# Optimization experiments

Measured on AMD Instinct MI355X. Metric: run time of the kernel, lower is better.

The kernel has to match this reference:

```python
import jax, jax.numpy as jnp
import numpy as np

IM_SIZE = (32, 32)
SCALE = float(IM_SIZE[0] * IM_SIZE[1])  # sqrt((x*y)^2) = x*y


def setup_inputs() -> dict:
    key = jax.random.key(0)
    k1, k2, k3 = jax.random.split(key, 3)
    b, n, p, x, y, d = 8, 8, 64, IM_SIZE[0], IM_SIZE[1], 8
    shape = (b, n, p, x, y, d)
    return {
        "query": jax.random.normal(k1, shape, dtype=jnp.float32),
        "key": jax.random.normal(k2, shape, dtype=jnp.float32),
        "value": jax.random.normal(k3, shape, dtype=jnp.float32),
        "key_padding_mask": jnp.zeros((b, p), dtype=bool),
    }


def reference(query, key, value, key_padding_mask):
    # scores: contract over spatial (x,y) and channel (d) dims -> [b,n,p,q]
    scores = jnp.einsum('bnpxyd,bnqxyd->bnpq', query, key) / SCALE
    if key_padding_mask is not None:
        mask = key_padding_mask[:, None, None, :]  # [b,1,1,q]
        scores = jnp.where(mask, -jnp.inf, scores)
    attn = jax.nn.softmax(scores, axis=-1)  # [b,n,p,q]
    out = jnp.einsum('bnpq,bnqxyd->bnpxyd', attn, value)
    # permute(0,2,3,4,5,1) -> [b,p,x,y,d,n]
    return jnp.transpose(out, (0, 2, 3, 4, 5, 1))
```

## Files before the change

### kernel.cpp

```cpp
#include <hip/hip_runtime.h>
#include <hip/hip_bf16.h>
#include <cstdint>
#include <cstddef>


typedef __attribute__((ext_vector_type(4))) float f32x4;
typedef __attribute__((ext_vector_type(8))) short bf16x8;
typedef __attribute__((ext_vector_type(4))) short shortx4;

__device__ __forceinline__ unsigned short f2bf(float x) {
    unsigned int u = __builtin_bit_cast(unsigned int, x);
    u += 0x7FFFu + ((u >> 16) & 1u);
    return (unsigned short)(u >> 16);
}

__global__ __launch_bounds__(256) void qk_mfma_kernel(
    const float* __restrict__ Q, const float* __restrict__ K,
    float* __restrict__ partial, int clen)
{
    const int bn   = blockIdx.x;
    const int ch   = blockIdx.y;
    const int tid  = threadIdx.x;
    const int w    = tid >> 6;
    const int lane = tid & 63;
    const int wr   = w >> 1;
    const int wc   = w & 1;
    const int frow = lane & 15;
    const int kg   = lane >> 4;

    const float* Qb = Q + (size_t)bn * 64 * 8192 + (size_t)ch * clen;
    const float* Kb = K + (size_t)bn * 64 * 8192 + (size_t)ch * clen;
    const float* Aq = Qb + (size_t)(wr * 32 + frow) * 8192 + kg * 8;
    const float* Bk = Kb + (size_t)(wc * 32 + frow) * 8192 + kg * 8;

    f32x4 acc[2][2];
    #pragma unroll
    for (int mt = 0; mt < 2; ++mt)
        #pragma unroll
        for (int nt = 0; nt < 2; ++nt)
            acc[mt][nt] = (f32x4)(0.f);

    #pragma unroll 2
    for (int ks = 0; ks < clen; ks += 32) {
        bf16x8 afr[2], bfr[2];
        #pragma unroll
        for (int mt = 0; mt < 2; ++mt) {
            const float* p = Aq + (size_t)mt * 16 * 8192 + ks;
            const float4 lo = *(const float4*)p;
            const float4 hi = *(const float4*)(p + 4);
            bf16x8 f;
            f[0] = (short)f2bf(lo.x); f[1] = (short)f2bf(lo.y);
            f[2] = (short)f2bf(lo.z); f[3] = (short)f2bf(lo.w);
            f[4] = (short)f2bf(hi.x); f[5] = (short)f2bf(hi.y);
            f[6] = (short)f2bf(hi.z); f[7] = (short)f2bf(hi.w);
            afr[mt] = f;
        }
        #pragma unroll
        for (int nt = 0; nt < 2; ++nt) {
            const float* p = Bk + (size_t)nt * 16 * 8192 + ks;
            const float4 lo = *(const float4*)p;
            const float4 hi = *(const float4*)(p + 4);
            bf16x8 f;
            f[0] = (short)f2bf(lo.x); f[1] = (short)f2bf(lo.y);
            f[2] = (short)f2bf(lo.z); f[3] = (short)f2bf(lo.w);
            f[4] = (short)f2bf(hi.x); f[5] = (short)f2bf(hi.y);
            f[6] = (short)f2bf(hi.z); f[7] = (short)f2bf(hi.w);
            bfr[nt] = f;
        }
        #pragma unroll
        for (int mt = 0; mt < 2; ++mt)
            #pragma unroll
            for (int nt = 0; nt < 2; ++nt)
                acc[mt][nt] = __builtin_amdgcn_mfma_f32_16x16x32_bf16(
                    afr[mt], bfr[nt], acc[mt][nt], 0, 0, 0);
    }

    float* pb = partial + ((size_t)ch * 64 + bn) * 4096;
    #pragma unroll
    for (int mt = 0; mt < 2; ++mt)
        #pragma unroll
        for (int nt = 0; nt < 2; ++nt) {
            const int p0 = wr * 32 + mt * 16 + kg * 4;
            const int q0 = wc * 32 + nt * 16 + frow;
            #pragma unroll
            for (int r = 0; r < 4; ++r)
                pb[(size_t)(p0 + r) * 64 + q0] = acc[mt][nt][r];
        }
}

__global__ __launch_bounds__(256) void softmax_kernel(
    float* __restrict__ ws, const unsigned char* __restrict__ mask, int kchunks)
{
    const int row  = blockIdx.x * 4 + (threadIdx.x >> 6);
    const int q    = threadIdx.x & 63;
    float s = 0.f;
    for (int c = 0; c < kchunks; ++c)
        s += ws[((size_t)c * 4096 + row) * 64 + q];
    s *= (1.0f / 1024.0f);
    const int b = row >> 9;
    if (mask[b * 64 + q]) s = -__builtin_inff();
    float m = s;
    #pragma unroll
    for (int off = 32; off; off >>= 1) m = fmaxf(m, __shfl_xor(m, off));
    const float e = __expf(s - m);
    float sum = e;
    #pragma unroll
    for (int off = 32; off; off >>= 1) sum += __shfl_xor(sum, off);
    ws[(size_t)row * 64 + q] = e / sum;
}

__global__ __launch_bounds__(512, 2) void pv_mfma_kernel(
    const float* __restrict__ V, const float* __restrict__ attn,
    float* __restrict__ out)
{
    __shared__ unsigned char smem[65536];

    const int b     = blockIdx.y;
    const int chunk = blockIdx.x;
    const int tid   = threadIdx.x;
    const int w     = tid >> 6;
    const int lane  = tid & 63;

    const float* Vb = V    + (size_t)(b * 8 + w) * 64 * 8192 + (size_t)chunk * 64;
    const float* Ab = attn + (size_t)(b * 8 + w) * 4096;

    unsigned short* vtn = (unsigned short*)smem + w * 4096;

    const int c  = lane >> 2;
    const int qg = lane & 3;
    #pragma unroll
    for (int s = 0; s < 4; ++s) {
        const int q0 = s * 16 + qg * 4;
        const float4 r0 = *(const float4*)&Vb[(size_t)(q0 + 0) * 8192 + c * 4];
        const float4 r1 = *(const float4*)&Vb[(size_t)(q0 + 1) * 8192 + c * 4];
        const float4 r2 = *(const float4*)&Vb[(size_t)(q0 + 2) * 8192 + c * 4];
        const float4 r3 = *(const float4*)&Vb[(size_t)(q0 + 3) * 8192 + c * 4];
        const float v0[4] = {r0.x, r0.y, r0.z, r0.w};
        const float v1[4] = {r1.x, r1.y, r1.z, r1.w};
        const float v2[4] = {r2.x, r2.y, r2.z, r2.w};
        const float v3[4] = {r3.x, r3.y, r3.z, r3.w};
        #pragma unroll
        for (int cc = 0; cc < 4; ++cc) {
            const int row = c * 4 + cc;
            shortx4 pk;
            pk.x = (short)f2bf(v0[cc]);
            pk.y = (short)f2bf(v1[cc]);
            pk.z = (short)f2bf(v2[cc]);
            pk.w = (short)f2bf(v3[cc]);
            const int soff = row * 64 + (q0 ^ ((row & 7) << 3) ^ (((row >> 3) & 3) << 4));
            *(shortx4*)(vtn + soff) = pk;
        }
    }

    const int arow = lane & 15;
    const int q0a  = (lane >> 4) * 8;
    bf16x8 afrag[4][2];
    #pragma unroll
    for (int mt = 0; mt < 4; ++mt) {
        #pragma unroll
        for (int ks = 0; ks < 2; ++ks) {
            const float* ap = Ab + (mt * 16 + arow) * 64 + ks * 32 + q0a;
            const float4 lo = *(const float4*)ap;
            const float4 hi = *(const float4*)(ap + 4);
            bf16x8 f;
            f[0] = (short)f2bf(lo.x); f[1] = (short)f2bf(lo.y);
            f[2] = (short)f2bf(lo.z); f[3] = (short)f2bf(lo.w);
            f[4] = (short)f2bf(hi.x); f[5] = (short)f2bf(hi.y);
            f[6] = (short)f2bf(hi.z); f[7] = (short)f2bf(hi.w);
            afrag[mt][ks] = f;
        }
    }

    f32x4 acc[4][4];
    #pragma unroll
    for (int mt = 0; mt < 4; ++mt)
        #pragma unroll
        for (int nt = 0; nt < 4; ++nt)
            acc[mt][nt] = (f32x4)(0.f);

    const int bcol = lane & 15;
    const int q0b  = (lane >> 4) * 8;
    #pragma unroll
    for (int nt = 0; nt < 4; ++nt) {
        bf16x8 bfr[2];
        #pragma unroll
        for (int ks = 0; ks < 2; ++ks) {
            const int row  = nt * 16 + bcol;
            const int q0   = ks * 32 + q0b;
            const int soff = row * 64 + (q0 ^ ((row & 7) << 3) ^ (((row >> 3) & 3) << 4));
            bfr[ks] = *(const bf16x8*)(vtn + soff);
        }
        #pragma unroll
        for (int ks = 0; ks < 2; ++ks)
            #pragma unroll
            for (int mt = 0; mt < 4; ++mt)
                acc[mt][nt] = __builtin_amdgcn_mfma_f32_16x16x32_bf16(
                    afrag[mt][ks], bfr[ks], acc[mt][nt], 0, 0, 0);
    }

    float* ob = (float*)smem;
    const int pq = lane >> 4;
    const int pl = tid >> 5;
    const int g  = tid & 31;
    #pragma unroll
    for (int mt = 0; mt < 4; ++mt) {
        __syncthreads();
        #pragma unroll
        for (int nt = 0; nt < 4; ++nt)
            #pragma unroll
            for (int r = 0; r < 4; ++r) {
                const int prow = pq * 4 + r;
                const int xc   = nt * 16 + (lane & 15);
                ob[prow * 576 + xc * 9 + w] = acc[mt][nt][r];
            }
        __syncthreads();
        float* orow = out + (size_t)b * 4194304 + (size_t)(mt * 16 + pl) * 65536
                          + (size_t)chunk * 512;
        #pragma unroll
        for (int u = 0; u < 4; ++u) {
            const int f0 = g * 4 + u * 128;
            float4 vv;
            vv.x = ob[pl * 576 + ((f0 + 0) >> 3) * 9 + ((f0 + 0) & 7)];
            vv.y = ob[pl * 576 + ((f0 + 1) >> 3) * 9 + ((f0 + 1) & 7)];
            vv.z = ob[pl * 576 + ((f0 + 2) >> 3) * 9 + ((f0 + 2) & 7)];
            vv.w = ob[pl * 576 + ((f0 + 3) >> 3) * 9 + ((f0 + 3) & 7)];
            *(float4*)&orow[f0] = vv;
        }
    }
}

extern "C" void kernel_launch(void* const* d_in, const int* in_sizes, int n_in,
                              void* d_out, int out_size, void* d_ws, size_t ws_size,
                              hipStream_t stream)
{
    const float* Q = (const float*)d_in[0];
    const float* K = (const float*)d_in[1];
    const float* V = (const float*)d_in[2];
    const unsigned char* mask = (const unsigned char*)d_in[3];
    float* out = (float*)d_out;
    float* ws  = (float*)d_ws;

    int kchunks = 16;
    while (kchunks > 1 &&
           (size_t)kchunks * 4096 * 64 * sizeof(float) > ws_size)
        kchunks >>= 1;
    const int clen = 8192 / kchunks;

    qk_mfma_kernel<<<dim3(64, kchunks), 256, 0, stream>>>(Q, K, ws, clen);
    softmax_kernel<<<1024, 256, 0, stream>>>(ws, mask, kchunks);
    pv_mfma_kernel<<<dim3(128, 8), 512, 0, stream>>>(V, ws, out);
}
```

Baseline: 152.5 us.

## Stage QK operands through double-buffered LDS with async global-to-LDS loads

The QK score kernel now copies Q and K tiles into a double-buffered shared-memory tile using global_load_lds (direct global-to-LDS DMA) with an XOR swizzle. It prefetches the next k-step while MFMAs run on the current one. Before this, each wave loaded strided rows straight from global memory, duplicating loads across waves and leaving latency exposed. The change adds a barrier per step and uses a lot of LDS, which may reduce occupancy. A small pack8 helper is also factored out.

Result: faster. 148.3 us (-2.8%).

```diff
diff --git a/kernel.cpp b/kernel.cpp
--- a/kernel.cpp
+++ b/kernel.cpp
@@ -14,10 +14,29 @@
     return (unsigned short)(u >> 16);
 }
 
+__device__ __forceinline__ bf16x8 pack8(float4 lo, float4 hi) {
+    bf16x8 f;
+    f[0] = (short)f2bf(lo.x); f[1] = (short)f2bf(lo.y);
+    f[2] = (short)f2bf(lo.z); f[3] = (short)f2bf(lo.w);
+    f[4] = (short)f2bf(hi.x); f[5] = (short)f2bf(hi.y);
+    f[6] = (short)f2bf(hi.z); f[7] = (short)f2bf(hi.w);
+    return f;
+}
+
+__device__ __forceinline__ void gload16(const float* g,
+    __attribute__((address_space(3))) float* l)
+{
+    __builtin_amdgcn_global_load_lds(
+        (const __attribute__((address_space(1))) unsigned int*)(uintptr_t)g,
+        (__attribute__((address_space(3))) unsigned int*)l, 16, 0, 0);
+}
+
 __global__ __launch_bounds__(256) void qk_mfma_kernel(
     const float* __restrict__ Q, const float* __restrict__ K,
     float* __restrict__ partial, int clen)
 {
+    __shared__ float tile[2][2][2048];
+
     const int bn   = blockIdx.x;
     const int ch   = blockIdx.y;
     const int tid  = threadIdx.x;
@@ -30,8 +49,23 @@
 
     const float* Qb = Q + (size_t)bn * 64 * 8192 + (size_t)ch * clen;
     const float* Kb = K + (size_t)bn * 64 * 8192 + (size_t)ch * clen;
-    const float* Aq = Qb + (size_t)(wr * 32 + frow) * 8192 + kg * 8;
-    const float* Bk = Kb + (size_t)(wc * 32 + frow) * 8192 + kg * 8;
+
+    auto lds3 = (__attribute__((address_space(3))) float*)(uintptr_t)&tile[0][0][0];
+
+    const int nsteps = clen >> 5;
+
+#define STAGE(db, t) do {                                                     \
+        _Pragma("unroll")                                                     \
+        for (int h = 0; h < 2; ++h) {                                         \
+            const int fi  = h * 256 + tid;                        \
+            const int row = fi >> 3;                                          \
+            const int ss  = (fi & 7) ^ (row & 7);   \
+            const float* gq = Qb + (size_t)row * 8192 + (size_t)(t) * 32 + ss * 4; \
+            const float* gk = Kb + (size_t)row * 8192 + (size_t)(t) * 32 + ss * 4; \
+            gload16(gq, lds3 + ((db) * 2 + 0) * 2048 + fi * 4);               \
+            gload16(gk, lds3 + ((db) * 2 + 1) * 2048 + fi * 4);               \
+        }                                                                     \
+    } while (0)
 
     f32x4 acc[2][2];
     #pragma unroll
@@ -40,40 +74,39 @@
         for (int nt = 0; nt < 2; ++nt)
             acc[mt][nt] = (f32x4)(0.f);
 
-    #pragma unroll 2
-    for (int ks = 0; ks < clen; ks += 32) {
+    const int f7 = frow & 7;
+    const int s0 = ((kg << 1)    ) ^ f7;
+    const int s1 = ((kg << 1) | 1) ^ f7;
+
+    STAGE(0, 0);
+    __syncthreads();
+
+    #pragma unroll 1
+    for (int t = 0; t < nsteps; ++t) {
+        const int db = t & 1;
+        if (t + 1 < nsteps) STAGE(db ^ 1, t + 1);
+
         bf16x8 afr[2], bfr[2];
         #pragma unroll
         for (int mt = 0; mt < 2; ++mt) {
-            const float* p = Aq + (size_t)mt * 16 * 8192 + ks;
-            const float4 lo = *(const float4*)p;
-            const float4 hi = *(const float4*)(p + 4);
-            bf16x8 f;
-            f[0] = (short)f2bf(lo.x); f[1] = (short)f2bf(lo.y);
-            f[2] = (short)f2bf(lo.z); f[3] = (short)f2bf(lo.w);
-            f[4] = (short)f2bf(hi.x); f[5] = (short)f2bf(hi.y);
-            f[6] = (short)f2bf(hi.z); f[7] = (short)f2bf(hi.w);
-            afr[mt] = f;
+            const float* base = &tile[db][0][(wr * 32 + mt * 16 + frow) * 32];
+            afr[mt] = pack8(*(const float4*)(base + s0 * 4),
+                            *(const float4*)(base + s1 * 4));
         }
         #pragma unroll
         for (int nt = 0; nt < 2; ++nt) {
-            const float* p = Bk + (size_t)nt * 16 * 8192 + ks;
-            const float4 lo = *(const float4*)p;
-            const float4 hi = *(const float4*)(p + 4);
-            bf16x8 f;
-            f[0] = (short)f2bf(lo.x); f[1] = (short)f2bf(lo.y);
-            f[2] = (short)f2bf(lo.z); f[3] = (short)f2bf(lo.w);
-            f[4] = (short)f2bf(hi.x); f[5] = (short)f2bf(hi.y);
-            f[6] = (short)f2bf(hi.z); f[7] = (short)f2bf(hi.w);
-            bfr[nt] = f;
-        }
-        #pragma unroll
-        for (int mt = 0; mt < 2; ++mt)
-            #pragma unroll
-            for (int nt = 0; nt < 2; ++nt)
-                acc[mt][nt] = __builtin_amdgcn_mfma_f32_16x16x32_bf16(
-                    afr[mt], bfr[nt], acc[mt][nt], 0, 0, 0);
-    }
+            const float* base = &tile[db][1][(wc * 32 + nt * 16 + frow) * 32];
+            bfr[nt] = pack8(*(const float4*)(base + s0 * 4),
+                            *(const float4*)(base + s1 * 4));
+        }
+        acc[0][0] = __builtin_amdgcn_mfma_f32_16x16x32_bf16(afr[0], bfr[0], acc[0][0], 0, 0, 0);
+        acc[0][1] = __builtin_amdgcn_mfma_f32_16x16x32_bf16(afr[0], bfr[1], acc[0][1], 0, 0, 0);
+        acc[1][0] = __builtin_amdgcn_mfma_f32_16x16x32_bf16(afr[1], bfr[0], acc[1][0], 0, 0, 0);
+        acc[1][1] = __builtin_amdgcn_mfma_f32_16x16x32_bf16(afr[1], bfr[1], acc[1][1], 0, 0, 0);
+
+        __syncthreads();
+    }
+#undef STAGE
 
     float* pb = partial + ((size_t)ch * 64 + bn) * 4096;
     #pragma unroll
@@ -162,12 +195,7 @@
             const float* ap = Ab + (mt * 16 + arow) * 64 + ks * 32 + q0a;
             const float4 lo = *(const float4*)ap;
             const float4 hi = *(const float4*)(ap + 4);
-            bf16x8 f;
-            f[0] = (short)f2bf(lo.x); f[1] = (short)f2bf(lo.y);
-            f[2] = (short)f2bf(lo.z); f[3] = (short)f2bf(lo.w);
-            f[4] = (short)f2bf(hi.x); f[5] = (short)f2bf(hi.y);
-            f[6] = (short)f2bf(hi.z); f[7] = (short)f2bf(hi.w);
-            afrag[mt][ks] = f;
+            afrag[mt][ks] = pack8(lo, hi);
         }
     }
 
```
